# Performance work log

Measured on AMD Instinct MI355X. Metric: run time of the kernel, lower is better.

The kernel has to match this reference:

```python
import jax, jax.numpy as jnp
import numpy as np

DIM = 256
HID = 256
EPS = 1e-5

def _layernorm(x, g, b):
    mu = jnp.mean(x, axis=-1, keepdims=True)
    var = jnp.mean(jnp.square(x - mu), axis=-1, keepdims=True)
    return (x - mu) * jax.lax.rsqrt(var + EPS) * g + b

def setup_inputs() -> dict:
    key = jax.random.key(0)
    ks = jax.random.split(key, 6)
    B, N = 2, 512
    x = jax.random.normal(ks[0], (B, N, DIM), dtype=jnp.float32)
    mask = jax.random.randint(ks[1], (B, N), 0, 2).astype(jnp.bool_)
    s_in = 1.0 / np.sqrt(DIM)
    s_h = 1.0 / np.sqrt(HID)
    return {
        "x": x,
        "mask": mask,
        "ln_g": jnp.ones((DIM,), jnp.float32),
        "ln_b": jnp.zeros((DIM,), jnp.float32),
        "Wl": jax.random.uniform(ks[2], (DIM, HID), jnp.float32, -s_in, s_in),
        "bl": jnp.zeros((HID,), jnp.float32),
        "Wo": jax.random.uniform(ks[3], (HID, HID), jnp.float32, -s_h, s_h),
        "bo": jnp.zeros((HID,), jnp.float32),
        "lno_g": jnp.ones((HID,), jnp.float32),
        "lno_b": jnp.zeros((HID,), jnp.float32),
    }

def reference(x, mask, ln_g, ln_b, Wl, bl, Wo, bo, lno_g, lno_b):
    # x: [B, N, D], mask: [B, N] bool
    xn = _layernorm(x, ln_g, ln_b)
    left = xn @ Wl + bl                                  # [B, N, H]
    outer = left[:, :, None, :] * left[:, None, :, :]    # [B, N, N, H]
    m2 = (mask[:, :, None] & mask[:, None, :])[..., None]  # [B, N, N, 1]
    outer = jnp.where(m2, outer, 0.0)
    h = _layernorm(jax.nn.gelu(outer, approximate=False), lno_g, lno_b)
    return h @ Wo + bo                                   # [B, N, N, H]
```

## Files before the change

### kernel.cpp

```cpp
#include <hip/hip_runtime.h>
#include <stdint.h>

#define DIM 256
#define HID 256
#define NSEQ 512
#define NB 2
#define EPS 1e-5f

typedef __attribute__((ext_vector_type(4))) float f32x4;
typedef __attribute__((ext_vector_type(4))) short bf16x4;
typedef __attribute__((ext_vector_type(8))) short bf16x8;

#define DIAG_BLOCKS 512
#define BATCH_BLOCKS 2304

__device__ __forceinline__ unsigned short f2bf(float f) {
    unsigned int u = __float_as_uint(f);
    u += 0x7fffu + ((u >> 16) & 1u);
    return (unsigned short)(u >> 16);
}

__device__ __forceinline__ float bfval(float f) {
    return __uint_as_float((unsigned)f2bf(f) << 16);
}

__device__ __forceinline__ float gelu_fast(float x) {
    const float z  = x * 0.7071067811865476f;
    const float az = fabsf(z);
    const float t  = __builtin_amdgcn_rcpf(fmaf(0.3275911f, az, 1.0f));
    float p = fmaf(1.061405429f, t, -1.453152027f);
    p = fmaf(p, t,  1.421413741f);
    p = fmaf(p, t, -0.284496736f);
    p = fmaf(p, t,  0.254829592f);
    p = p * t;
    const float e = __builtin_amdgcn_exp2f(az * az * -1.4426950408889634f);
    float erfv = fmaf(-p, e, 1.0f);
    erfv = copysignf(erfv, z);
    return 0.5f * x * (1.0f + erfv);
}

__device__ __forceinline__ int pairpos(int k) {
    return ((k >> 5) << 5) + (((k >> 2) & 3) << 3) + (((k >> 4) & 1) << 2) + (k & 3);
}

__global__ __launch_bounds__(256) void prep_kernel(
    const float* __restrict__ x, const void* __restrict__ mask,
    const float* __restrict__ ln_g, const float* __restrict__ ln_b,
    const float* __restrict__ Wl, const float* __restrict__ bl,
    const float* __restrict__ Wo, const float* __restrict__ lno_b,
    const float* __restrict__ bo,
    float* __restrict__ lm, unsigned short* __restrict__ woTp,
    int* __restrict__ maskr, float* __restrict__ cst)
{
    const int row = blockIdx.x;
    const int t = threadIdx.x;
    const int lane = t & 63, w = t >> 6;
    __shared__ float xs[DIM];
    __shared__ float red[8];
    __shared__ int bad_s[4];

    {
        const int v = ((const int*)mask)[t];
        unsigned long long bm = __ballot((v & ~1) != 0);
        if (lane == 0) bad_s[w] = (bm != 0ull) ? 1 : 0;
    }

    float v = x[row * DIM + t];
    float s = v, ss = v * v;
    #pragma unroll
    for (int o = 32; o; o >>= 1) { s += __shfl_xor(s, o); ss += __shfl_xor(ss, o); }
    if (lane == 0) { red[w] = s; red[4 + w] = ss; }
    __syncthreads();
    s  = red[0] + red[1] + red[2] + red[3];
    ss = red[4] + red[5] + red[6] + red[7];
    const float mu  = s * (1.0f / DIM);
    const float var = ss * (1.0f / DIM) - mu * mu;
    const float rs  = rsqrtf(var + EPS);
    xs[t] = (v - mu) * rs * ln_g[t] + ln_b[t];
    __syncthreads();

    float acc = bl[t];
    #pragma unroll 4
    for (int k = 0; k < DIM; k += 4) {
        float4 xv = *(const float4*)&xs[k];
        acc = fmaf(xv.x, Wl[(k + 0) * HID + t], acc);
        acc = fmaf(xv.y, Wl[(k + 1) * HID + t], acc);
        acc = fmaf(xv.z, Wl[(k + 2) * HID + t], acc);
        acc = fmaf(xv.w, Wl[(k + 3) * HID + t], acc);
    }
    const int packed = bad_s[0] | bad_s[1] | bad_s[2] | bad_s[3];
    const int mv = packed ? (int)((const unsigned char*)mask)[row]
                          : ((const int*)mask)[row];
    lm[row * HID + t] = mv ? acc : 0.0f;
    if (t == 0) maskr[row] = mv;

    if (row < HID) {
        woTp[row * HID + pairpos(t)] = f2bf(Wo[t * HID + row]);
    }
    if (row == 0) {
        float c = bo[t];
        for (int k = 0; k < HID; ++k)
            c = fmaf(bfval(lno_b[k]), bfval(Wo[k * HID + t]), c);
        cst[t] = c;
    }
}

__global__ __launch_bounds__(512) void outer_kernel(
    const float* __restrict__ lm, const unsigned short* __restrict__ woTp,
    const float* __restrict__ lno_g, const float* __restrict__ lno_b,
    const float* __restrict__ bo, const int* __restrict__ maskr,
    const float* __restrict__ cst, float* __restrict__ out)
{
    int blk = (int)blockIdx.x;
    int b = 0;
    if (blk >= BATCH_BLOCKS) { b = 1; blk -= BATCH_BLOCKS; }
    int i, jt, mirror;
    if (blk < DIAG_BLOCKS) {
        i = blk; jt = i >> 6; mirror = 0;
    } else {
        const int r2 = blk - DIAG_BLOCKS;
        const int p  = r2 >> 6;
        const int il = r2 & 63;
        int bi = 0, start = 0;
        #pragma unroll
        for (int bb = 0; bb < 7; ++bb) {
            const int s = bb * 7 - (bb * (bb - 1)) / 2;
            if (p >= s) { bi = bb; start = s; }
        }
        const int bj = bi + 1 + (p - start);
        i = bi * 64 + il;
        jt = bj;
        mirror = 1;
    }
    const int j0  = jt * 64;
    const int t    = threadIdx.x;
    const int lane = t & 63;
    const int w    = t >> 6;
    const size_t base = (size_t)(b * NSEQ + i) * NSEQ * HID;

    if (maskr[b * NSEQ + i] == 0) {
        const f32x4 c = *(const f32x4*)&cst[lane * 4];
        #pragma unroll
        for (int r = 0; r < 8; ++r) {
            const int j = j0 + w * 8 + r;
            *(f32x4*)&out[base + (size_t)j * HID + lane * 4] = c;
            if (mirror)
                *(f32x4*)&out[((size_t)(b * NSEQ + j) * NSEQ + i) * HID + lane * 4] = c;
        }
        return;
    }

    __shared__ __align__(16) unsigned char ybuf[64 * 512];

    const int n0  = w * 32;
    const int l15 = lane & 15;
    const int q   = lane >> 4;

    bf16x8 b8[16];
    #pragma unroll
    for (int kk2 = 0; kk2 < 8; ++kk2)
        #pragma unroll
        for (int nh = 0; nh < 2; ++nh)
            b8[kk2 * 2 + nh] =
                *(const bf16x8*)&woTp[(n0 + nh * 16 + l15) * HID + kk2 * 32 + q * 8];

    const float4 li4 = *(const float4*)&lm[(size_t)(b * NSEQ + i) * HID + lane * 4];
    const float4 g4  = *(const float4*)&lno_g[lane * 4];
    const float4 bb4 = *(const float4*)&lno_b[lane * 4];

    const int mvl = maskr[b * NSEQ + j0 + lane];
    const unsigned long long livemask = __ballot(mvl != 0);

    const int wrb = ((lane >> 3) << 6) + ((lane & 3) << 4) + (((lane >> 2) & 1) << 3);

    const uint2 ucst = make_uint2(
        ((unsigned)f2bf(bb4.y) << 16) | (unsigned)f2bf(bb4.x),
        ((unsigned)f2bf(bb4.w) << 16) | (unsigned)f2bf(bb4.z));

    #pragma unroll 4
    for (int r = 0; r < 8; ++r) {
        const int rl = w * 8 + r;
        const int j  = j0 + rl;
        const int off = rl * 512 + (wrb ^ ((rl & 7) << 4));
        if (!((livemask >> rl) & 1ull)) {
            *(uint2*)&ybuf[off] = ucst;
            continue;
        }
        float4 lj4 = *(const float4*)&lm[(size_t)(b * NSEQ + j) * HID + lane * 4];
        float4 p;
        p.x = gelu_fast(li4.x * lj4.x);
        p.y = gelu_fast(li4.y * lj4.y);
        p.z = gelu_fast(li4.z * lj4.z);
        p.w = gelu_fast(li4.w * lj4.w);
        float s  = p.x + p.y + p.z + p.w;
        float ss = p.x * p.x + p.y * p.y + p.z * p.z + p.w * p.w;
        #pragma unroll
        for (int o = 32; o; o >>= 1) { s += __shfl_xor(s, o); ss += __shfl_xor(ss, o); }
        const float mu  = s * (1.0f / HID);
        const float var = ss * (1.0f / HID) - mu * mu;
        const float rs  = rsqrtf(var + EPS);
        const float y0 = (p.x - mu) * rs * g4.x + bb4.x;
        const float y1 = (p.y - mu) * rs * g4.y + bb4.y;
        const float y2 = (p.z - mu) * rs * g4.z + bb4.z;
        const float y3 = (p.w - mu) * rs * g4.w + bb4.w;
        const unsigned int u0 = ((unsigned)f2bf(y1) << 16) | (unsigned)f2bf(y0);
        const unsigned int u1 = ((unsigned)f2bf(y3) << 16) | (unsigned)f2bf(y2);
        *(uint2*)&ybuf[off] = make_uint2(u0, u1);
    }
    __syncthreads();

    #pragma unroll
    for (int mi = 0; mi < 4; ++mi) {
        const int rowm  = mi * 16 + l15;
        const int rbyte = rowm * 512;
        const int swz   = (rowm & 7) << 4;

        f32x4 acc[2];
        acc[0] = (f32x4){0.f, 0.f, 0.f, 0.f};
        acc[1] = (f32x4){0.f, 0.f, 0.f, 0.f};

#if !__has_builtin(__builtin_amdgcn_mfma_f32_16x16x16bf16_1k)
        asm volatile("" : "+v"(acc[0]), "+v"(acc[1]));
        asm volatile("s_nop 1");
#endif

        #pragma unroll
        for (int kk2 = 0; kk2 < 8; ++kk2) {
            const bf16x8 a8 = *(const bf16x8*)&ybuf[rbyte + ((kk2 * 64 + q * 16) ^ swz)];
            const bf16x4 alo = __builtin_shufflevector(a8, a8, 0, 1, 2, 3);
            const bf16x4 ahi = __builtin_shufflevector(a8, a8, 4, 5, 6, 7);
            #pragma unroll
            for (int nh = 0; nh < 2; ++nh) {
                const bf16x8 bf8 = b8[kk2 * 2 + nh];
                const bf16x4 blo = __builtin_shufflevector(bf8, bf8, 0, 1, 2, 3);
                const bf16x4 bhi = __builtin_shufflevector(bf8, bf8, 4, 5, 6, 7);
#if __has_builtin(__builtin_amdgcn_mfma_f32_16x16x16bf16_1k)
                acc[nh] = __builtin_amdgcn_mfma_f32_16x16x16bf16_1k(
                    blo, alo, acc[nh], 0, 0, 0);
                acc[nh] = __builtin_amdgcn_mfma_f32_16x16x16bf16_1k(
                    bhi, ahi, acc[nh], 0, 0, 0);
#else
                asm volatile("v_mfma_f32_16x16x16_bf16 %0, %1, %2, %0"
                             : "+v"(acc[nh]) : "v"(blo), "v"(alo));
                asm volatile("v_mfma_f32_16x16x16_bf16 %0, %1, %2, %0"
                             : "+v"(acc[nh]) : "v"(bhi), "v"(ahi));
#endif
            }
        }

#if !__has_builtin(__builtin_amdgcn_mfma_f32_16x16x16bf16_1k)
        asm volatile("s_nop 7");
        asm volatile("s_nop 7");
        asm volatile("" : "+v"(acc[0]), "+v"(acc[1]));
#endif

        const int j = j0 + rowm;
        const size_t prow = base + (size_t)j * HID;
        const size_t mrow = ((size_t)(b * NSEQ + j) * NSEQ + i) * HID;
        #pragma unroll
        for (int nh = 0; nh < 2; ++nh) {
            const int h0 = n0 + nh * 16 + q * 4;
            const float4 bo4 = *(const float4*)&bo[h0];
            f32x4 o;
            o[0] = acc[nh][0] + bo4.x;
            o[1] = acc[nh][1] + bo4.y;
            o[2] = acc[nh][2] + bo4.z;
            o[3] = acc[nh][3] + bo4.w;
            *(f32x4*)&out[prow + h0] = o;
            if (mirror)
                *(f32x4*)&out[mrow + h0] = o;
        }
    }
}

extern "C" void kernel_launch(void* const* d_in, const int* in_sizes, int n_in,
                              void* d_out, int out_size, void* d_ws, size_t ws_size,
                              hipStream_t stream) {
    (void)in_sizes; (void)n_in; (void)out_size; (void)ws_size;
    const float* x     = (const float*)d_in[0];
    const void*  mask  = d_in[1];
    const float* ln_g  = (const float*)d_in[2];
    const float* ln_b  = (const float*)d_in[3];
    const float* Wl    = (const float*)d_in[4];
    const float* bl    = (const float*)d_in[5];
    const float* Wo    = (const float*)d_in[6];
    const float* bo    = (const float*)d_in[7];
    const float* lno_g = (const float*)d_in[8];
    const float* lno_b = (const float*)d_in[9];

    char* ws = (char*)d_ws;
    float*          lm    = (float*)ws;
    unsigned short* woTp  = (unsigned short*)(ws + (size_t)NB * NSEQ * HID * 4);
    int*            maskr = (int*)(ws + (size_t)NB * NSEQ * HID * 4 + HID * HID * 2);
    float*          cst   = (float*)(ws + (size_t)NB * NSEQ * HID * 4 + HID * HID * 2
                                        + NB * NSEQ * 4);

    prep_kernel<<<NB * NSEQ, 256, 0, stream>>>(x, mask, ln_g, ln_b, Wl, bl, Wo,
                                               lno_b, bo, lm, woTp, maskr, cst);
    outer_kernel<<<NB * BATCH_BLOCKS, 512, 0, stream>>>(
        lm, woTp, lno_g, lno_b, bo, maskr, cst, (float*)d_out);
}
```

Baseline: 155.0 us.

## Make outer kernel persistent with double-buffered LDS tile pipeline

Turns the outer kernel into a persistent kernel of 512 blocks, each working through 9 consecutive tiles. The Wo fragments and per-block constants are loaded once per block instead of once per tile. A two-slot LDS buffer lets the GELU/layernorm stage for the next tile run alongside the MFMA and store stage of the current tile. The risks are less parallelism (fewer blocks, 64KB of LDS per block) and load imbalance, since runs of masked tiles are no longer spread across separate blocks.

```diff
diff --git a/kernel.cpp b/kernel.cpp
--- a/kernel.cpp
+++ b/kernel.cpp
@@ -13,6 +13,9 @@
 
 #define DIAG_BLOCKS 512
 #define BATCH_BLOCKS 2304
+#define NTILES (NB * BATCH_BLOCKS)
+#define PBLOCKS 512
+#define TILES_PER_BLOCK (NTILES / PBLOCKS)
 
 __device__ __forceinline__ unsigned short f2bf(float f) {
     unsigned int u = __float_as_uint(f);
@@ -105,18 +108,15 @@
     }
 }
 
-__global__ __launch_bounds__(512) void outer_kernel(
-    const float* __restrict__ lm, const unsigned short* __restrict__ woTp,
-    const float* __restrict__ lno_g, const float* __restrict__ lno_b,
-    const float* __restrict__ bo, const int* __restrict__ maskr,
-    const float* __restrict__ cst, float* __restrict__ out)
-{
-    int blk = (int)blockIdx.x;
-    int b = 0;
-    if (blk >= BATCH_BLOCKS) { b = 1; blk -= BATCH_BLOCKS; }
-    int i, jt, mirror;
+struct Tile { int b, i, j0, mirror, live; size_t base; };
+
+__device__ __forceinline__ Tile decode_tile(int idx, const int* __restrict__ maskr) {
+    Tile tl;
+    int blk = idx;
+    tl.b = 0;
+    if (blk >= BATCH_BLOCKS) { tl.b = 1; blk -= BATCH_BLOCKS; }
     if (blk < DIAG_BLOCKS) {
-        i = blk; jt = i >> 6; mirror = 0;
+        tl.i = blk; tl.j0 = (tl.i >> 6) * 64; tl.mirror = 0;
     } else {
         const int r2 = blk - DIAG_BLOCKS;
         const int p  = r2 >> 6;
@@ -128,33 +128,40 @@
             if (p >= s) { bi = bb; start = s; }
         }
         const int bj = bi + 1 + (p - start);
-        i = bi * 64 + il;
-        jt = bj;
-        mirror = 1;
-    }
-    const int j0  = jt * 64;
+        tl.i = bi * 64 + il;
+        tl.j0 = bj * 64;
+        tl.mirror = 1;
+    }
+    tl.base = (size_t)(tl.b * NSEQ + tl.i) * NSEQ * HID;
+    tl.live = maskr[tl.b * NSEQ + tl.i] != 0;
+    return tl;
+}
+
+__global__ __launch_bounds__(512, 4) void outer_kernel(
+    const float* __restrict__ lm, const unsigned short* __restrict__ woTp,
+    const float* __restrict__ lno_g, const float* __restrict__ lno_b,
+    const float* __restrict__ bo, const int* __restrict__ maskr,
+    const float* __restrict__ cst, float* __restrict__ out)
+{
     const int t    = threadIdx.x;
     const int lane = t & 63;
     const int w    = t >> 6;
-    const size_t base = (size_t)(b * NSEQ + i) * NSEQ * HID;
-
-    if (maskr[b * NSEQ + i] == 0) {
-        const f32x4 c = *(const f32x4*)&cst[lane * 4];
-        #pragma unroll
-        for (int r = 0; r < 8; ++r) {
-            const int j = j0 + w * 8 + r;
-            *(f32x4*)&out[base + (size_t)j * HID + lane * 4] = c;
-            if (mirror)
-                *(f32x4*)&out[((size_t)(b * NSEQ + j) * NSEQ + i) * HID + lane * 4] = c;
-        }
-        return;
-    }
-
-    __shared__ __align__(16) unsigned char ybuf[64 * 512];
-
-    const int n0  = w * 32;
-    const int l15 = lane & 15;
-    const int q   = lane >> 4;
+    const int n0   = w * 32;
+    const int l15  = lane & 15;
+    const int q    = lane >> 4;
+
+    __shared__ __align__(16) unsigned char ybuf[2][64 * 512];
+
+    const float4 g4  = *(const float4*)&lno_g[lane * 4];
+    const float4 bb4 = *(const float4*)&lno_b[lane * 4];
+    const f32x4  cvec = *(const f32x4*)&cst[lane * 4];
+    const uint2 ucst = make_uint2(
+        ((unsigned)f2bf(bb4.y) << 16) | (unsigned)f2bf(bb4.x),
+        ((unsigned)f2bf(bb4.w) << 16) | (unsigned)f2bf(bb4.z));
+    const int wrb = ((lane >> 3) << 6) + ((lane & 3) << 4) + (((lane >> 2) & 1) << 3);
+    float4 bo4[2];
+    bo4[0] = *(const float4*)&bo[n0 + q * 4];
+    bo4[1] = *(const float4*)&bo[n0 + 16 + q * 4];
 
     bf16x8 b8[16];
     #pragma unroll
@@ -164,112 +171,128 @@
             b8[kk2 * 2 + nh] =
                 *(const bf16x8*)&woTp[(n0 + nh * 16 + l15) * HID + kk2 * 32 + q * 8];
 
-    const float4 li4 = *(const float4*)&lm[(size_t)(b * NSEQ + i) * HID + lane * 4];
-    const float4 g4  = *(const float4*)&lno_g[lane * 4];
-    const float4 bb4 = *(const float4*)&lno_b[lane * 4];
-
-    const int mvl = maskr[b * NSEQ + j0 + lane];
-    const unsigned long long livemask = __ballot(mvl != 0);
-
-    const int wrb = ((lane >> 3) << 6) + ((lane & 3) << 4) + (((lane >> 2) & 1) << 3);
-
-    const uint2 ucst = make_uint2(
-        ((unsigned)f2bf(bb4.y) << 16) | (unsigned)f2bf(bb4.x),
-        ((unsigned)f2bf(bb4.w) << 16) | (unsigned)f2bf(bb4.z));
-
-    #pragma unroll 4
-    for (int r = 0; r < 8; ++r) {
-        const int rl = w * 8 + r;
-        const int j  = j0 + rl;
-        const int off = rl * 512 + (wrb ^ ((rl & 7) << 4));
-        if (!((livemask >> rl) & 1ull)) {
-            *(uint2*)&ybuf[off] = ucst;
-            continue;
-        }
-        float4 lj4 = *(const float4*)&lm[(size_t)(b * NSEQ + j) * HID + lane * 4];
-        float4 p;
-        p.x = gelu_fast(li4.x * lj4.x);
-        p.y = gelu_fast(li4.y * lj4.y);
-        p.z = gelu_fast(li4.z * lj4.z);
-        p.w = gelu_fast(li4.w * lj4.w);
-        float s  = p.x + p.y + p.z + p.w;
-        float ss = p.x * p.x + p.y * p.y + p.z * p.z + p.w * p.w;
+    auto phaseA = [&](const Tile& tl, unsigned char* buf) {
+        const float4 li4 = *(const float4*)&lm[(size_t)(tl.b * NSEQ + tl.i) * HID + lane * 4];
+        const int mvl = maskr[tl.b * NSEQ + tl.j0 + lane];
+        const unsigned long long livemask = __ballot(mvl != 0);
+        #pragma unroll 4
+        for (int r = 0; r < 8; ++r) {
+            const int rl = w * 8 + r;
+            const int off = rl * 512 + (wrb ^ ((rl & 7) << 4));
+            if (!((livemask >> rl) & 1ull)) {
+                *(uint2*)&buf[off] = ucst;
+                continue;
+            }
+            const int j = tl.j0 + rl;
+            float4 lj4 = *(const float4*)&lm[(size_t)(tl.b * NSEQ + j) * HID + lane * 4];
+            float4 p;
+            p.x = gelu_fast(li4.x * lj4.x);
+            p.y = gelu_fast(li4.y * lj4.y);
+            p.z = gelu_fast(li4.z * lj4.z);
+            p.w = gelu_fast(li4.w * lj4.w);
+            float s  = p.x + p.y + p.z + p.w;
+            float ss = p.x * p.x + p.y * p.y + p.z * p.z + p.w * p.w;
+            #pragma unroll
+            for (int o = 32; o; o >>= 1) { s += __shfl_xor(s, o); ss += __shfl_xor(ss, o); }
+            const float mu  = s * (1.0f / HID);
+            const float var = ss * (1.0f / HID) - mu * mu;
+            const float rs  = rsqrtf(var + EPS);
+            const float y0 = (p.x - mu) * rs * g4.x + bb4.x;
+            const float y1 = (p.y - mu) * rs * g4.y + bb4.y;
+            const float y2 = (p.z - mu) * rs * g4.z + bb4.z;
+            const float y3 = (p.w - mu) * rs * g4.w + bb4.w;
+            const unsigned int u0 = ((unsigned)f2bf(y1) << 16) | (unsigned)f2bf(y0);
+            const unsigned int u1 = ((unsigned)f2bf(y3) << 16) | (unsigned)f2bf(y2);
+            *(uint2*)&buf[off] = make_uint2(u0, u1);
+        }
+    };
+
+    auto phaseB = [&](const Tile& tl, const unsigned char* buf) {
         #pragma unroll
-        for (int o = 32; o; o >>= 1) { s += __shfl_xor(s, o); ss += __shfl_xor(ss, o); }
-        const float mu  = s * (1.0f / HID);
-        const float var = ss * (1.0f / HID) - mu * mu;
-        const float rs  = rsqrtf(var + EPS);
-        const float y0 = (p.x - mu) * rs * g4.x + bb4.x;
-        const float y1 = (p.y - mu) * rs * g4.y + bb4.y;
-        const float y2 = (p.z - mu) * rs * g4.z + bb4.z;
-        const float y3 = (p.w - mu) * rs * g4.w + bb4.w;
-        const unsigned int u0 = ((unsigned)f2bf(y1) << 16) | (unsigned)f2bf(y0);
-        const unsigned int u1 = ((unsigned)f2bf(y3) << 16) | (unsigned)f2bf(y2);
-        *(uint2*)&ybuf[off] = make_uint2(u0, u1);
-    }
-    __syncthreads();
-
-    #pragma unroll
-    for (int mi = 0; mi < 4; ++mi) {
-        const int rowm  = mi * 16 + l15;
-        const int rbyte = rowm * 512;
-        const int swz   = (rowm & 7) << 4;
-
-        f32x4 acc[2];
-        acc[0] = (f32x4){0.f, 0.f, 0.f, 0.f};
-        acc[1] = (f32x4){0.f, 0.f, 0.f, 0.f};
+        for (int mi = 0; mi < 4; ++mi) {
+            const int rowm  = mi * 16 + l15;
+            const int rbyte = rowm * 512;
+            const int swz   = (rowm & 7) << 4;
+
+            f32x4 acc[2];
+            acc[0] = (f32x4){0.f, 0.f, 0.f, 0.f};
+            acc[1] = (f32x4){0.f, 0.f, 0.f, 0.f};
+
+            #pragma unroll
+            for (int kk2 = 0; kk2 < 8; ++kk2) {
+                const bf16x8 a8 = *(const bf16x8*)&buf[rbyte + ((kk2 * 64 + q * 16) ^ swz)];
+                const bf16x4 alo = __builtin_shufflevector(a8, a8, 0, 1, 2, 3);
+                const bf16x4 ahi = __builtin_shufflevector(a8, a8, 4, 5, 6, 7);
+                #pragma unroll
+                for (int nh = 0; nh < 2; ++nh) {
+                    const bf16x8 bf8 = b8[kk2 * 2 + nh];
+                    const bf16x4 blo = __builtin_shufflevector(bf8, bf8, 0, 1, 2, 3);
+                    const bf16x4 bhi = __builtin_shufflevector(bf8, bf8, 4, 5, 6, 7);
+#if __has_builtin(__builtin_amdgcn_mfma_f32_16x16x16bf16_1k)
+                    acc[nh] = __builtin_amdgcn_mfma_f32_16x16x16bf16_1k(
+                        blo, alo, acc[nh], 0, 0, 0);
+                    acc[nh] = __builtin_amdgcn_mfma_f32_16x16x16bf16_1k(
+                        bhi, ahi, acc[nh], 0, 0, 0);
+#else
+                    asm volatile("v_mfma_f32_16x16x16_bf16 %0, %1, %2, %0"
+                                 : "+v"(acc[nh]) : "v"(blo), "v"(alo));
+                    asm volatile("v_mfma_f32_16x16x16_bf16 %0, %1, %2, %0"
+                                 : "+v"(acc[nh]) : "v"(bhi), "v"(ahi));
+#endif
+                }
+            }
 
 #if !__has_builtin(__builtin_amdgcn_mfma_f32_16x16x16bf16_1k)
-        asm volatile("" : "+v"(acc[0]), "+v"(acc[1]));
-        asm volatile("s_nop 1");
+            asm volatile("s_nop 7");
+            asm volatile("s_nop 7");
+            asm volatile("" : "+v"(acc[0]), "+v"(acc[1]));
 #endif
 
-        #pragma unroll
-        for (int kk2 = 0; kk2 < 8; ++kk2) {
-            const bf16x8 a8 = *(const bf16x8*)&ybuf[rbyte + ((kk2 * 64 + q * 16) ^ swz)];
-            const bf16x4 alo = __builtin_shufflevector(a8, a8, 0, 1, 2, 3);
-            const bf16x4 ahi = __builtin_shufflevector(a8, a8, 4, 5, 6, 7);
+            const int j = tl.j0 + rowm;
+            const size_t prow = tl.base + (size_t)j * HID;
+            const size_t mrow = ((size_t)(tl.b * NSEQ + j) * NSEQ + tl.i) * HID;
             #pragma unroll
             for (int nh = 0; nh < 2; ++nh) {
-                const bf16x8 bf8 = b8[kk2 * 2 + nh];
-                const bf16x4 blo = __builtin_shufflevector(bf8, bf8, 0, 1, 2, 3);
-                const bf16x4 bhi = __builtin_shufflevector(bf8, bf8, 4, 5, 6, 7);
-#if __has_builtin(__builtin_amdgcn_mfma_f32_16x16x16bf16_1k)
-                acc[nh] = __builtin_amdgcn_mfma_f32_16x16x16bf16_1k(
-                    blo, alo, acc[nh], 0, 0, 0);
-                acc[nh] = __builtin_amdgcn_mfma_f32_16x16x16bf16_1k(
-                    bhi, ahi, acc[nh], 0, 0, 0);
-#else
-                asm volatile("v_mfma_f32_16x16x16_bf16 %0, %1, %2, %0"
-                             : "+v"(acc[nh]) : "v"(blo), "v"(alo));
-                asm volatile("v_mfma_f32_16x16x16_bf16 %0, %1, %2, %0"
-                             : "+v"(acc[nh]) : "v"(bhi), "v"(ahi));
-#endif
+                const int h0 = n0 + nh * 16 + q * 4;
+                f32x4 o;
+                o[0] = acc[nh][0] + bo4[nh].x;
+                o[1] = acc[nh][1] + bo4[nh].y;
+                o[2] = acc[nh][2] + bo4[nh].z;
+                o[3] = acc[nh][3] + bo4[nh].w;
+                *(f32x4*)&out[prow + h0] = o;
+                if (tl.mirror)
+                    *(f32x4*)&out[mrow + h0] = o;
             }
         }
-
-#if !__has_builtin(__builtin_amdgcn_mfma_f32_16x16x16bf16_1k)
-        asm volatile("s_nop 7");
-        asm volatile("s_nop 7");
-        asm volatile("" : "+v"(acc[0]), "+v"(acc[1]));
-#endif
-
-        const int j = j0 + rowm;
-        const size_t prow = base + (size_t)j * HID;
-        const size_t mrow = ((size_t)(b * NSEQ + j) * NSEQ + i) * HID;
+    };
+
+    auto deadB = [&](const Tile& tl) {
         #pragma unroll
-        for (int nh = 0; nh < 2; ++nh) {
-            const int h0 = n0 + nh * 16 + q * 4;
-            const float4 bo4 = *(const float4*)&bo[h0];
-            f32x4 o;
-            o[0] = acc[nh][0] + bo4.x;
-            o[1] = acc[nh][1] + bo4.y;
-            o[2] = acc[nh][2] + bo4.z;
-            o[3] = acc[nh][3] + bo4.w;
-            *(f32x4*)&out[prow + h0] = o;
-            if (mirror)
-                *(f32x4*)&out[mrow + h0] = o;
-        }
+        for (int r = 0; r < 8; ++r) {
+            const int j = tl.j0 + w * 8 + r;
+            *(f32x4*)&out[tl.base + (size_t)j * HID + lane * 4] = cvec;
+            if (tl.mirror)
+                *(f32x4*)&out[((size_t)(tl.b * NSEQ + j) * NSEQ + tl.i) * HID + lane * 4] = cvec;
+        }
+    };
+
+    const int tile0 = (int)blockIdx.x * TILES_PER_BLOCK;
+
+    Tile cur = decode_tile(tile0, maskr);
+    if (cur.live) phaseA(cur, ybuf[0]);
+    __syncthreads();
+
+    for (int tt = 0; tt < TILES_PER_BLOCK; ++tt) {
+        if (cur.live) phaseB(cur, ybuf[tt & 1]);
+        else          deadB(cur);
+
+        Tile nxt;
+        if (tt + 1 < TILES_PER_BLOCK) {
+            nxt = decode_tile(tile0 + tt + 1, maskr);
+            if (nxt.live) phaseA(nxt, ybuf[(tt + 1) & 1]);
+        }
+        __syncthreads();
+        cur = nxt;
     }
 }
 
@@ -297,6 +320,6 @@
 
     prep_kernel<<<NB * NSEQ, 256, 0, stream>>>(x, mask, ln_g, ln_b, Wl, bl, Wo,
                                                lno_b, bo, lm, woTp, maskr, cst);
-    outer_kernel<<<NB * BATCH_BLOCKS, 512, 0, stream>>>(
+    outer_kernel<<<PBLOCKS, 512, 0, stream>>>(
         lm, woTp, lno_g, lno_b, bo, maskr, cst, (float*)d_out);
 }
```

New measurement: 182.6 us. +17.9%, slower.
